# Kernel optimization log

Measured on AMD Instinct MI355X. Metric: run time of the kernel, lower is better.

The kernel has to match this reference:

```python
import jax, jax.numpy as jnp
import numpy as np

E, TOP_K, H, I = 8, 2, 1024, 2048
B, S = 1, 2048


def setup_inputs() -> dict:
    key = jax.random.key(0)
    ks = jax.random.split(key, 5)
    scale_h = 1.0 / np.sqrt(H)
    scale_i = 1.0 / np.sqrt(I)
    return {
        "hidden_states": jax.random.normal(ks[0], (B, S, H), dtype=jnp.float32),
        "gate_w": jax.random.normal(ks[1], (E, H), dtype=jnp.float32) * scale_h,
        "w1": jax.random.normal(ks[2], (E, I, H), dtype=jnp.float32) * scale_h,
        "w3": jax.random.normal(ks[3], (E, I, H), dtype=jnp.float32) * scale_h,
        "w2": jax.random.normal(ks[4], (E, H, I), dtype=jnp.float32) * scale_i,
    }


def _moe(x, gate_w, w1, w3, w2):
    orig_shape = x.shape
    xt = x.reshape(-1, H)                       # [T, H]
    logits = xt @ gate_w.T                      # [T, E] router logits
    probs = jax.nn.softmax(logits, axis=-1)
    topw, topi = jax.lax.top_k(probs, TOP_K)    # [T, K]
    topw = topw / jnp.sum(topw, axis=-1, keepdims=True)  # renormalize=True
    # dense per-token expert weights [T, E]
    ew = jnp.sum(jax.nn.one_hot(topi, E, dtype=xt.dtype) * topw[..., None], axis=1)
    # SwiGLU experts, vectorized over all experts
    g = jnp.einsum('th,eih->tei', xt, w1)       # [T, E, I]
    u = jnp.einsum('th,eih->tei', xt, w3)
    act = jax.nn.silu(g) * u
    ye = jnp.einsum('tei,ehi->teh', act, w2)    # [T, E, H]
    out = jnp.einsum('te,teh->th', ew, ye)      # weighted combine
    return out.reshape(orig_shape)


def reference(hidden_states, gate_w, w1, w3, w2):
    return _moe(hidden_states, gate_w, w1, w3, w2)
```

## Files before the change

kernel.cpp:

```cpp
#include <hip/hip_runtime.h>
#include <hip/hip_bf16.h>
#include <math.h>

#define T_TOK 2048
#define HD 1024
#define ID 2048
#define NE 8
#define LDT 72

typedef __attribute__((ext_vector_type(8))) short s16x8;
typedef __attribute__((ext_vector_type(8))) unsigned short u16x8;
typedef __attribute__((ext_vector_type(4))) float f32x4;
typedef __attribute__((ext_vector_type(4))) unsigned short u16x4;

__device__ __forceinline__ unsigned short f2bf(float f) {
  union { float f; unsigned u; } v; v.f = f;
  unsigned r = v.u + 0x7FFFu + ((v.u >> 16) & 1u);
  return (unsigned short)(r >> 16);
}

__device__ __forceinline__ u16x8 pack8(float4 a, float4 b) {
  u16x8 v;
  v[0] = f2bf(a.x); v[1] = f2bf(a.y); v[2] = f2bf(a.z); v[3] = f2bf(a.w);
  v[4] = f2bf(b.x); v[5] = f2bf(b.y); v[6] = f2bf(b.z); v[7] = f2bf(b.w);
  return v;
}

__device__ __forceinline__ void lgkm_barrier() {
  asm volatile("s_waitcnt lgkmcnt(0)" ::: "memory");
  __builtin_amdgcn_s_barrier();
}

#define GLOAD16(gsrc, ldst) \
  __builtin_amdgcn_global_load_lds((const __attribute__((address_space(1))) void*)(gsrc), \
                                   (__attribute__((address_space(3))) void*)(ldst), 16, 0, 0)

__global__ void router_k(const float* __restrict__ x, const float* __restrict__ gate,
                         int* __restrict__ cnt, int* __restrict__ tok,
                         float* __restrict__ wt, int* __restrict__ inv) {
  int wid = threadIdx.x >> 6, lane = threadIdx.x & 63;
  int t = blockIdx.x * 4 + wid;
  const float* xr = x + (size_t)t * HD;
  float acc[NE];
#pragma unroll
  for (int e = 0; e < NE; e++) acc[e] = 0.f;
  for (int h = lane; h < HD; h += 64) {
    float xv = xr[h];
#pragma unroll
    for (int e = 0; e < NE; e++) acc[e] += xv * gate[e * HD + h];
  }
#pragma unroll
  for (int e = 0; e < NE; e++)
    for (int off = 32; off; off >>= 1) acc[e] += __shfl_xor(acc[e], off);
  int i0 = 0;
#pragma unroll
  for (int e = 1; e < NE; e++) if (acc[e] > acc[i0]) i0 = e;
  int i1 = (i0 == 0) ? 1 : 0;
#pragma unroll
  for (int e = 0; e < NE; e++) if (e != i0 && acc[e] > acc[i1]) i1 = e;
  float w0 = 1.f / (1.f + expf(acc[i1] - acc[i0]));
  float w1 = 1.f - w0;
  if (lane == 0) {
    int p0 = atomicAdd(&cnt[i0], 1);
    tok[i0 * T_TOK + p0] = t; wt[i0 * T_TOK + p0] = w0;
    inv[2 * t] = (i0 << 16) | p0;
    int p1 = atomicAdd(&cnt[i1], 1);
    tok[i1 * T_TOK + p1] = t; wt[i1 * T_TOK + p1] = w1;
    inv[2 * t + 1] = (i1 << 16) | p1;
  }
}

__global__ void prefix_k(const int* __restrict__ cnt, int* __restrict__ offs) {
  if (threadIdx.x == 0) {
    int s = 0;
    for (int e = 0; e < NE; e++) { offs[e] = s; s += cnt[e]; }
  }
}

__global__ void gather_k(const float* __restrict__ x, const int* __restrict__ cnt,
                         const int* __restrict__ offs, const int* __restrict__ tok,
                         unsigned short* __restrict__ Xg) {
  int e = blockIdx.x >> 11, slot = blockIdx.x & 2047;
  if (slot >= cnt[e]) return;
  int t = tok[e * T_TOK + slot];
  int row = offs[e] + slot;
  int c = threadIdx.x * 4;
  float4 f = *(const float4*)(x + (size_t)t * HD + c);
  u16x4 o; o.x = f2bf(f.x); o.y = f2bf(f.y); o.z = f2bf(f.z); o.w = f2bf(f.w);
  *(u16x4*)(Xg + (size_t)row * HD + c) = o;
}

__global__ __launch_bounds__(256, 3) void gemm1_k(
    const unsigned short* __restrict__ Xg, const float* __restrict__ w1,
    const float* __restrict__ w3, const int* __restrict__ cnt,
    const int* __restrict__ offs, const float* __restrict__ wt,
    unsigned short* __restrict__ act) {
  int e = blockIdx.z;
  int count = cnt[e];
  int mt = blockIdx.y;
  if (mt * 128 >= count) return;
  int i0 = blockIdx.x * 64;
  int rbase = offs[e] + mt * 128;
  const float* W1 = w1 + (size_t)e * ID * HD;
  const float* W3 = w3 + (size_t)e * ID * HD;

  __shared__ __align__(16) unsigned short Abuf[2][128 * 64];
  __shared__ __align__(16) unsigned short B1s[64 * LDT];
  __shared__ __align__(16) unsigned short B2s[64 * LDT];

  int tid = threadIdx.x;
  int wid = tid >> 6, lane = tid & 63;
  int wr = wid >> 1, wc = wid & 1;
  int l15 = lane & 15, hi = lane >> 4;
  int br = tid >> 2, bc = (tid & 3) * 16;

  int swz_col = ((lane & 7) ^ (lane >> 3)) * 8;
  const unsigned short* ag[4];
#pragma unroll
  for (int c = 0; c < 4; c++)
    ag[c] = Xg + (size_t)(rbase + c * 32 + wid * 8 + (lane >> 3)) * HD + swz_col;

  const float* s1 = W1 + (size_t)(i0 + br) * HD + bc;
  const float* s2 = W3 + (size_t)(i0 + br) * HD + bc;

  f32x4 accg[4][2], accu[4][2];
#pragma unroll
  for (int m = 0; m < 4; m++)
#pragma unroll
    for (int n = 0; n < 2; n++) {
      accg[m][n] = (f32x4){0.f, 0.f, 0.f, 0.f};
      accu[m][n] = (f32x4){0.f, 0.f, 0.f, 0.f};
    }

#pragma unroll
  for (int c = 0; c < 4; c++) GLOAD16(ag[c], &Abuf[0][c * 2048 + wid * 512]);
  float4 p1[4], p2[4];
#pragma unroll
  for (int j = 0; j < 4; j++) { p1[j] = *(const float4*)(s1 + j * 4); p2[j] = *(const float4*)(s2 + j * 4); }

  for (int t = 0; t < 16; ++t) {
    int cur = t & 1;
    lgkm_barrier();
    *(u16x8*)&B1s[br * LDT + bc]     = pack8(p1[0], p1[1]);
    *(u16x8*)&B1s[br * LDT + bc + 8] = pack8(p1[2], p1[3]);
    *(u16x8*)&B2s[br * LDT + bc]     = pack8(p2[0], p2[1]);
    *(u16x8*)&B2s[br * LDT + bc + 8] = pack8(p2[2], p2[3]);
    lgkm_barrier();
    __builtin_amdgcn_sched_barrier(0);
    if (t < 15) {
      int k0n = (t + 1) * 64;
#pragma unroll
      for (int c = 0; c < 4; c++)
        GLOAD16(ag[c] + k0n, &Abuf[cur ^ 1][c * 2048 + wid * 512]);
#pragma unroll
      for (int j = 0; j < 4; j++) {
        p1[j] = *(const float4*)(s1 + k0n + j * 4);
        p2[j] = *(const float4*)(s2 + k0n + j * 4);
      }
    }
#pragma unroll
    for (int kk = 0; kk < 2; ++kk) {
      s16x8 a[4], b1[2], b2[2];
#pragma unroll
      for (int m = 0; m < 4; m++) {
        int r = wr * 64 + m * 16 + l15;
        a[m] = *(const s16x8*)&Abuf[cur][r * 64 + (((kk * 4 + hi) ^ (r & 7)) * 8)];
      }
#pragma unroll
      for (int n = 0; n < 2; n++) {
        b1[n] = *(const s16x8*)&B1s[(wc * 32 + n * 16 + l15) * LDT + kk * 32 + hi * 8];
        b2[n] = *(const s16x8*)&B2s[(wc * 32 + n * 16 + l15) * LDT + kk * 32 + hi * 8];
      }
#pragma unroll
      for (int m = 0; m < 4; m++)
#pragma unroll
        for (int n = 0; n < 2; n++) {
          accg[m][n] = __builtin_amdgcn_mfma_f32_16x16x32_bf16(a[m], b1[n], accg[m][n], 0, 0, 0);
          accu[m][n] = __builtin_amdgcn_mfma_f32_16x16x32_bf16(a[m], b2[n], accu[m][n], 0, 0, 0);
        }
    }
  }

#pragma unroll
  for (int m = 0; m < 4; m++)
#pragma unroll
    for (int r = 0; r < 4; r++) {
      int rl = mt * 128 + wr * 64 + m * 16 + (lane >> 4) * 4 + r;
      if (rl < count) {
        float w = wt[e * T_TOK + rl];
#pragma unroll
        for (int n = 0; n < 2; n++) {
          float g = accg[m][n][r], u = accu[m][n][r];
          float s = (g / (1.f + expf(-g))) * u * w;
          act[(size_t)(offs[e] + rl) * ID + i0 + wc * 32 + n * 16 + l15] = f2bf(s);
        }
      }
    }
}

__global__ __launch_bounds__(256, 3) void gemm2_k(
    const unsigned short* __restrict__ act, const float* __restrict__ w2,
    const int* __restrict__ cnt, const int* __restrict__ offs,
    float* __restrict__ ye) {
  int e = blockIdx.z;
  int count = cnt[e];
  int mt = blockIdx.y;
  if (mt * 128 >= count) return;
  int h0 = blockIdx.x * 64;
  int rbase = offs[e] + mt * 128;
  const float* W2 = w2 + (size_t)e * HD * ID;

  __shared__ __align__(16) unsigned short Abuf[2][128 * 64];
  __shared__ __align__(16) unsigned short Bs[64 * LDT];

  int tid = threadIdx.x;
  int wid = tid >> 6, lane = tid & 63;
  int wr = wid >> 1, wc = wid & 1;
  int l15 = lane & 15, hi = lane >> 4;
  int br = tid >> 2, bc = (tid & 3) * 16;

  int swz_col = ((lane & 7) ^ (lane >> 3)) * 8;
  const unsigned short* ag[4];
#pragma unroll
  for (int c = 0; c < 4; c++)
    ag[c] = act + (size_t)(rbase + c * 32 + wid * 8 + (lane >> 3)) * ID + swz_col;

  const float* sb = W2 + (size_t)(h0 + br) * ID + bc;

  f32x4 acc[4][2];
#pragma unroll
  for (int m = 0; m < 4; m++)
#pragma unroll
    for (int n = 0; n < 2; n++) acc[m][n] = (f32x4){0.f, 0.f, 0.f, 0.f};

#pragma unroll
  for (int c = 0; c < 4; c++) GLOAD16(ag[c], &Abuf[0][c * 2048 + wid * 512]);
  float4 pb[4];
#pragma unroll
  for (int j = 0; j < 4; j++) pb[j] = *(const float4*)(sb + j * 4);

  for (int t = 0; t < 32; ++t) {
    int cur = t & 1;
    lgkm_barrier();
    *(u16x8*)&Bs[br * LDT + bc]     = pack8(pb[0], pb[1]);
    *(u16x8*)&Bs[br * LDT + bc + 8] = pack8(pb[2], pb[3]);
    lgkm_barrier();
    __builtin_amdgcn_sched_barrier(0);
    if (t < 31) {
      int k0n = (t + 1) * 64;
#pragma unroll
      for (int c = 0; c < 4; c++)
        GLOAD16(ag[c] + k0n, &Abuf[cur ^ 1][c * 2048 + wid * 512]);
#pragma unroll
      for (int j = 0; j < 4; j++) pb[j] = *(const float4*)(sb + k0n + j * 4);
    }
#pragma unroll
    for (int kk = 0; kk < 2; ++kk) {
      s16x8 a[4], b[2];
#pragma unroll
      for (int m = 0; m < 4; m++) {
        int r = wr * 64 + m * 16 + l15;
        a[m] = *(const s16x8*)&Abuf[cur][r * 64 + (((kk * 4 + hi) ^ (r & 7)) * 8)];
      }
#pragma unroll
      for (int n = 0; n < 2; n++)
        b[n] = *(const s16x8*)&Bs[(wc * 32 + n * 16 + l15) * LDT + kk * 32 + hi * 8];
#pragma unroll
      for (int m = 0; m < 4; m++)
#pragma unroll
        for (int n = 0; n < 2; n++)
          acc[m][n] = __builtin_amdgcn_mfma_f32_16x16x32_bf16(a[m], b[n], acc[m][n], 0, 0, 0);
    }
  }

#pragma unroll
  for (int m = 0; m < 4; m++)
#pragma unroll
    for (int r = 0; r < 4; r++) {
      int slot = mt * 128 + wr * 64 + m * 16 + (lane >> 4) * 4 + r;
      if (slot < count) {
#pragma unroll
        for (int n = 0; n < 2; n++)
          ye[(size_t)(offs[e] + slot) * HD + h0 + wc * 32 + n * 16 + l15] = acc[m][n][r];
      }
    }
}

__global__ void combine_k(const float* __restrict__ ye, const int* __restrict__ inv,
                          const int* __restrict__ offs, float* __restrict__ out) {
  int t = blockIdx.x;
  int c = threadIdx.x * 4;
  int v0 = inv[2 * t], v1 = inv[2 * t + 1];
  int r0 = offs[v0 >> 16] + (v0 & 0xFFFF);
  int r1 = offs[v1 >> 16] + (v1 & 0xFFFF);
  float4 a = *(const float4*)(ye + (size_t)r0 * HD + c);
  float4 b = *(const float4*)(ye + (size_t)r1 * HD + c);
  float4 o = {a.x + b.x, a.y + b.y, a.z + b.z, a.w + b.w};
  *(float4*)(out + (size_t)t * HD + c) = o;
}

extern "C" void kernel_launch(void* const* d_in, const int* in_sizes, int n_in,
                              void* d_out, int out_size, void* d_ws, size_t ws_size,
                              hipStream_t stream) {
  const float* x    = (const float*)d_in[0];
  const float* gate = (const float*)d_in[1];
  const float* w1   = (const float*)d_in[2];
  const float* w3   = (const float*)d_in[3];
  const float* w2   = (const float*)d_in[4];
  float* out = (float*)d_out;

  char* ws = (char*)d_ws;
  int* cnt  = (int*)(ws + 0);
  int* offs = (int*)(ws + 256);
  int* tok  = (int*)(ws + 512);
  float* wt = (float*)(ws + 66048);
  int* inv  = (int*)(ws + 131584);
  unsigned short* Xg  = (unsigned short*)(ws + 148480);
  unsigned short* act = (unsigned short*)(ws + 8799232);
  float* ye = (float*)(ws + 26100736);

  hipMemsetAsync(cnt, 0, 256, stream);

  router_k<<<T_TOK / 4, 256, 0, stream>>>(x, gate, cnt, tok, wt, inv);
  prefix_k<<<1, 64, 0, stream>>>(cnt, offs);
  gather_k<<<NE * T_TOK, 256, 0, stream>>>(x, cnt, offs, tok, Xg);
  gemm1_k<<<dim3(ID / 64, 16, NE), 256, 0, stream>>>(Xg, w1, w3, cnt, offs, wt, act);
  gemm2_k<<<dim3(HD / 64, 16, NE), 256, 0, stream>>>(act, w2, cnt, offs, ye);
  combine_k<<<T_TOK, 256, 0, stream>>>(ye, inv, offs, out);
}
```

Before: 371.1 us.

## Stream fp32 expert weights into LDS asynchronously and enlarge M tiles

Both expert GEMMs now move fp32 weight tiles straight into shared memory with asynchronous global-to-LDS loads, using an XOR swizzle, and convert them to bf16 when the fragments are read. Previously the weights went through registers and were packed to bf16 before an LDS store. Blocks grow to 512 threads covering 256 token rows with a K step of 32, and the grid is flattened with experts interleaved in the block index. Each weight tile is therefore re-read fewer times and the register round trip leaves the inner loop. In exchange each wave converts fp32 to bf16 redundantly, barriers become more frequent, and the grid assumes at most 1024 tokens per expert.

```diff
diff --git a/kernel.cpp b/kernel.cpp
--- a/kernel.cpp
+++ b/kernel.cpp
@@ -6,7 +6,6 @@
 #define HD 1024
 #define ID 2048
 #define NE 8
-#define LDT 72
 
 typedef __attribute__((ext_vector_type(8))) short s16x8;
 typedef __attribute__((ext_vector_type(8))) unsigned short u16x8;
@@ -19,21 +18,22 @@
   return (unsigned short)(r >> 16);
 }
 
-__device__ __forceinline__ u16x8 pack8(float4 a, float4 b) {
-  u16x8 v;
-  v[0] = f2bf(a.x); v[1] = f2bf(a.y); v[2] = f2bf(a.z); v[3] = f2bf(a.w);
-  v[4] = f2bf(b.x); v[5] = f2bf(b.y); v[6] = f2bf(b.z); v[7] = f2bf(b.w);
-  return v;
-}
-
-__device__ __forceinline__ void lgkm_barrier() {
-  asm volatile("s_waitcnt lgkmcnt(0)" ::: "memory");
-  __builtin_amdgcn_s_barrier();
+__device__ __forceinline__ s16x8 cvt8(float4 a, float4 b) {
+  union { s16x8 v; __hip_bfloat16 h[8]; } u;
+  u.h[0] = __float2bfloat16(a.x); u.h[1] = __float2bfloat16(a.y);
+  u.h[2] = __float2bfloat16(a.z); u.h[3] = __float2bfloat16(a.w);
+  u.h[4] = __float2bfloat16(b.x); u.h[5] = __float2bfloat16(b.y);
+  u.h[6] = __float2bfloat16(b.z); u.h[7] = __float2bfloat16(b.w);
+  return u.v;
 }
 
 #define GLOAD16(gsrc, ldst) \
   __builtin_amdgcn_global_load_lds((const __attribute__((address_space(1))) void*)(gsrc), \
                                    (__attribute__((address_space(3))) void*)(ldst), 16, 0, 0)
+
+#define WAIT_BARRIER() do { \
+  asm volatile("s_waitcnt vmcnt(0) lgkmcnt(0)" ::: "memory"); \
+  __builtin_amdgcn_s_barrier(); } while (0)
 
 __global__ void router_k(const float* __restrict__ x, const float* __restrict__ gate,
                          int* __restrict__ cnt, int* __restrict__ tok,
@@ -90,38 +90,40 @@
   *(u16x4*)(Xg + (size_t)row * HD + c) = o;
 }
 
-__global__ __launch_bounds__(256, 3) void gemm1_k(
+__global__ __launch_bounds__(512, 4) void gemm1_k(
     const unsigned short* __restrict__ Xg, const float* __restrict__ w1,
     const float* __restrict__ w3, const int* __restrict__ cnt,
     const int* __restrict__ offs, const float* __restrict__ wt,
     unsigned short* __restrict__ act) {
-  int e = blockIdx.z;
+  int bid = blockIdx.x;
+  int e = bid & 7;
+  int r2 = bid >> 3;
+  int nt = r2 & 31, mt = r2 >> 5;
   int count = cnt[e];
-  int mt = blockIdx.y;
-  if (mt * 128 >= count) return;
-  int i0 = blockIdx.x * 64;
-  int rbase = offs[e] + mt * 128;
+  if (mt * 256 >= count) return;
+  int i0 = nt * 64;
+  int rbase = offs[e] + mt * 256;
   const float* W1 = w1 + (size_t)e * ID * HD;
   const float* W3 = w3 + (size_t)e * ID * HD;
 
-  __shared__ __align__(16) unsigned short Abuf[2][128 * 64];
-  __shared__ __align__(16) unsigned short B1s[64 * LDT];
-  __shared__ __align__(16) unsigned short B2s[64 * LDT];
+  __shared__ __align__(16) unsigned short Ab[2][256 * 32];
+  __shared__ __align__(16) float B1b[2][64 * 32];
+  __shared__ __align__(16) float B2b[2][64 * 32];
 
   int tid = threadIdx.x;
   int wid = tid >> 6, lane = tid & 63;
   int wr = wid >> 1, wc = wid & 1;
   int l15 = lane & 15, hi = lane >> 4;
-  int br = tid >> 2, bc = (tid & 3) * 16;
-
-  int swz_col = ((lane & 7) ^ (lane >> 3)) * 8;
-  const unsigned short* ag[4];
-#pragma unroll
-  for (int c = 0; c < 4; c++)
-    ag[c] = Xg + (size_t)(rbase + c * 32 + wid * 8 + (lane >> 3)) * HD + swz_col;
-
-  const float* s1 = W1 + (size_t)(i0 + br) * HD + bc;
-  const float* s2 = W3 + (size_t)(i0 + br) * HD + bc;
+
+  const unsigned short* aS[2];
+#pragma unroll
+  for (int c = 0; c < 2; c++)
+    aS[c] = Xg + (size_t)(rbase + c * 128 + wid * 16 + (lane >> 2)) * HD
+               + (((lane & 3) ^ ((lane >> 2) & 3)) * 8);
+  const float* b1S = W1 + (size_t)(i0 + wid * 8 + (lane >> 3)) * HD
+                        + (((lane & 7) ^ ((lane >> 3) & 7)) * 4);
+  const float* b2S = W3 + (size_t)(i0 + wid * 8 + (lane >> 3)) * HD
+                        + (((lane & 7) ^ ((lane >> 3) & 7)) * 4);
 
   f32x4 accg[4][2], accu[4][2];
 #pragma unroll
@@ -132,100 +134,92 @@
       accu[m][n] = (f32x4){0.f, 0.f, 0.f, 0.f};
     }
 
-#pragma unroll
-  for (int c = 0; c < 4; c++) GLOAD16(ag[c], &Abuf[0][c * 2048 + wid * 512]);
-  float4 p1[4], p2[4];
-#pragma unroll
-  for (int j = 0; j < 4; j++) { p1[j] = *(const float4*)(s1 + j * 4); p2[j] = *(const float4*)(s2 + j * 4); }
-
-  for (int t = 0; t < 16; ++t) {
+  int aswz = (hi ^ (l15 & 3)) * 8;
+  int bg0 = ((hi * 2) ^ (l15 & 7)) * 4;
+  int bg1 = ((hi * 2 + 1) ^ (l15 & 7)) * 4;
+
+#define G1_STAGE(buf, k0) do { \
+    GLOAD16(aS[0] + (k0), &Ab[buf][wid * 512]); \
+    GLOAD16(aS[1] + (k0), &Ab[buf][4096 + wid * 512]); \
+    GLOAD16(b1S + (k0), &B1b[buf][wid * 256]); \
+    GLOAD16(b2S + (k0), &B2b[buf][wid * 256]); } while (0)
+
+  G1_STAGE(0, 0);
+  WAIT_BARRIER();
+
+  for (int t = 0; t < 32; ++t) {
     int cur = t & 1;
-    lgkm_barrier();
-    *(u16x8*)&B1s[br * LDT + bc]     = pack8(p1[0], p1[1]);
-    *(u16x8*)&B1s[br * LDT + bc + 8] = pack8(p1[2], p1[3]);
-    *(u16x8*)&B2s[br * LDT + bc]     = pack8(p2[0], p2[1]);
-    *(u16x8*)&B2s[br * LDT + bc + 8] = pack8(p2[2], p2[3]);
-    lgkm_barrier();
-    __builtin_amdgcn_sched_barrier(0);
-    if (t < 15) {
-      int k0n = (t + 1) * 64;
-#pragma unroll
-      for (int c = 0; c < 4; c++)
-        GLOAD16(ag[c] + k0n, &Abuf[cur ^ 1][c * 2048 + wid * 512]);
-#pragma unroll
-      for (int j = 0; j < 4; j++) {
-        p1[j] = *(const float4*)(s1 + k0n + j * 4);
-        p2[j] = *(const float4*)(s2 + k0n + j * 4);
+    if (t < 31) G1_STAGE(cur ^ 1, (t + 1) * 32);
+    s16x8 a[4];
+#pragma unroll
+    for (int m = 0; m < 4; m++)
+      a[m] = *(const s16x8*)&Ab[cur][(wr * 64 + m * 16 + l15) * 32 + aswz];
+#pragma unroll
+    for (int n = 0; n < 2; n++) {
+      int rB = (wc * 32 + n * 16 + l15) * 32;
+      float4 q0 = *(const float4*)&B1b[cur][rB + bg0];
+      float4 q1 = *(const float4*)&B1b[cur][rB + bg1];
+      s16x8 b1 = cvt8(q0, q1);
+      float4 q2 = *(const float4*)&B2b[cur][rB + bg0];
+      float4 q3 = *(const float4*)&B2b[cur][rB + bg1];
+      s16x8 b2 = cvt8(q2, q3);
+#pragma unroll
+      for (int m = 0; m < 4; m++) {
+        accg[m][n] = __builtin_amdgcn_mfma_f32_16x16x32_bf16(a[m], b1, accg[m][n], 0, 0, 0);
+        accu[m][n] = __builtin_amdgcn_mfma_f32_16x16x32_bf16(a[m], b2, accu[m][n], 0, 0, 0);
       }
     }
-#pragma unroll
-    for (int kk = 0; kk < 2; ++kk) {
-      s16x8 a[4], b1[2], b2[2];
-#pragma unroll
-      for (int m = 0; m < 4; m++) {
-        int r = wr * 64 + m * 16 + l15;
-        a[m] = *(const s16x8*)&Abuf[cur][r * 64 + (((kk * 4 + hi) ^ (r & 7)) * 8)];
-      }
-#pragma unroll
-      for (int n = 0; n < 2; n++) {
-        b1[n] = *(const s16x8*)&B1s[(wc * 32 + n * 16 + l15) * LDT + kk * 32 + hi * 8];
-        b2[n] = *(const s16x8*)&B2s[(wc * 32 + n * 16 + l15) * LDT + kk * 32 + hi * 8];
-      }
-#pragma unroll
-      for (int m = 0; m < 4; m++)
-#pragma unroll
-        for (int n = 0; n < 2; n++) {
-          accg[m][n] = __builtin_amdgcn_mfma_f32_16x16x32_bf16(a[m], b1[n], accg[m][n], 0, 0, 0);
-          accu[m][n] = __builtin_amdgcn_mfma_f32_16x16x32_bf16(a[m], b2[n], accu[m][n], 0, 0, 0);
-        }
-    }
+    WAIT_BARRIER();
   }
 
 #pragma unroll
   for (int m = 0; m < 4; m++)
 #pragma unroll
     for (int r = 0; r < 4; r++) {
-      int rl = mt * 128 + wr * 64 + m * 16 + (lane >> 4) * 4 + r;
+      int rl = mt * 256 + wr * 64 + m * 16 + hi * 4 + r;
       if (rl < count) {
         float w = wt[e * T_TOK + rl];
 #pragma unroll
         for (int n = 0; n < 2; n++) {
           float g = accg[m][n][r], u = accu[m][n][r];
           float s = (g / (1.f + expf(-g))) * u * w;
-          act[(size_t)(offs[e] + rl) * ID + i0 + wc * 32 + n * 16 + l15] = f2bf(s);
+          act[(size_t)(offs[e] + rl) * ID + i0 + wc * 32 + n * 16 + l15] =
+              (unsigned short)__bfloat16_as_ushort(__float2bfloat16(s));
         }
       }
     }
-}
-
-__global__ __launch_bounds__(256, 3) void gemm2_k(
+#undef G1_STAGE
+}
+
+__global__ __launch_bounds__(512, 4) void gemm2_k(
     const unsigned short* __restrict__ act, const float* __restrict__ w2,
     const int* __restrict__ cnt, const int* __restrict__ offs,
     float* __restrict__ ye) {
-  int e = blockIdx.z;
+  int bid = blockIdx.x;
+  int e = bid & 7;
+  int r2 = bid >> 3;
+  int nt = r2 & 15, mt = r2 >> 4;
   int count = cnt[e];
-  int mt = blockIdx.y;
-  if (mt * 128 >= count) return;
-  int h0 = blockIdx.x * 64;
-  int rbase = offs[e] + mt * 128;
+  if (mt * 256 >= count) return;
+  int h0 = nt * 64;
+  int rbase = offs[e] + mt * 256;
   const float* W2 = w2 + (size_t)e * HD * ID;
 
-  __shared__ __align__(16) unsigned short Abuf[2][128 * 64];
-  __shared__ __align__(16) unsigned short Bs[64 * LDT];
+  __shared__ __align__(16) unsigned short Ab[2][256 * 32];
+  __shared__ __align__(16) float Bb[2][64 * 32];
 
   int tid = threadIdx.x;
   int wid = tid >> 6, lane = tid & 63;
   int wr = wid >> 1, wc = wid & 1;
   int l15 = lane & 15, hi = lane >> 4;
-  int br = tid >> 2, bc = (tid & 3) * 16;
-
-  int swz_col = ((lane & 7) ^ (lane >> 3)) * 8;
-  const unsigned short* ag[4];
-#pragma unroll
-  for (int c = 0; c < 4; c++)
-    ag[c] = act + (size_t)(rbase + c * 32 + wid * 8 + (lane >> 3)) * ID + swz_col;
-
-  const float* sb = W2 + (size_t)(h0 + br) * ID + bc;
+
+  const unsigned short* aS[2];
+#pragma unroll
+  for (int c = 0; c < 2; c++)
+    aS[c] = act + (size_t)(rbase + c * 128 + wid * 16 + (lane >> 2)) * ID
+                + (((lane & 3) ^ ((lane >> 2) & 3)) * 8);
+  const float* bS = W2 + (size_t)(h0 + wid * 8 + (lane >> 3)) * ID
+                       + (((lane & 7) ^ ((lane >> 3) & 7)) * 4);
 
   f32x4 acc[4][2];
 #pragma unroll
@@ -233,57 +227,50 @@
 #pragma unroll
     for (int n = 0; n < 2; n++) acc[m][n] = (f32x4){0.f, 0.f, 0.f, 0.f};
 
-#pragma unroll
-  for (int c = 0; c < 4; c++) GLOAD16(ag[c], &Abuf[0][c * 2048 + wid * 512]);
-  float4 pb[4];
-#pragma unroll
-  for (int j = 0; j < 4; j++) pb[j] = *(const float4*)(sb + j * 4);
-
-  for (int t = 0; t < 32; ++t) {
+  int aswz = (hi ^ (l15 & 3)) * 8;
+  int bg0 = ((hi * 2) ^ (l15 & 7)) * 4;
+  int bg1 = ((hi * 2 + 1) ^ (l15 & 7)) * 4;
+
+#define G2_STAGE(buf, k0) do { \
+    GLOAD16(aS[0] + (k0), &Ab[buf][wid * 512]); \
+    GLOAD16(aS[1] + (k0), &Ab[buf][4096 + wid * 512]); \
+    GLOAD16(bS + (k0), &Bb[buf][wid * 256]); } while (0)
+
+  G2_STAGE(0, 0);
+  WAIT_BARRIER();
+
+  for (int t = 0; t < 64; ++t) {
     int cur = t & 1;
-    lgkm_barrier();
-    *(u16x8*)&Bs[br * LDT + bc]     = pack8(pb[0], pb[1]);
-    *(u16x8*)&Bs[br * LDT + bc + 8] = pack8(pb[2], pb[3]);
-    lgkm_barrier();
-    __builtin_amdgcn_sched_barrier(0);
-    if (t < 31) {
-      int k0n = (t + 1) * 64;
-#pragma unroll
-      for (int c = 0; c < 4; c++)
-        GLOAD16(ag[c] + k0n, &Abuf[cur ^ 1][c * 2048 + wid * 512]);
-#pragma unroll
-      for (int j = 0; j < 4; j++) pb[j] = *(const float4*)(sb + k0n + j * 4);
-    }
-#pragma unroll
-    for (int kk = 0; kk < 2; ++kk) {
-      s16x8 a[4], b[2];
-#pragma unroll
-      for (int m = 0; m < 4; m++) {
-        int r = wr * 64 + m * 16 + l15;
-        a[m] = *(const s16x8*)&Abuf[cur][r * 64 + (((kk * 4 + hi) ^ (r & 7)) * 8)];
-      }
-#pragma unroll
-      for (int n = 0; n < 2; n++)
-        b[n] = *(const s16x8*)&Bs[(wc * 32 + n * 16 + l15) * LDT + kk * 32 + hi * 8];
+    if (t < 63) G2_STAGE(cur ^ 1, (t + 1) * 32);
+    s16x8 a[4];
+#pragma unroll
+    for (int m = 0; m < 4; m++)
+      a[m] = *(const s16x8*)&Ab[cur][(wr * 64 + m * 16 + l15) * 32 + aswz];
+#pragma unroll
+    for (int n = 0; n < 2; n++) {
+      int rB = (wc * 32 + n * 16 + l15) * 32;
+      float4 q0 = *(const float4*)&Bb[cur][rB + bg0];
+      float4 q1 = *(const float4*)&Bb[cur][rB + bg1];
+      s16x8 b = cvt8(q0, q1);
 #pragma unroll
       for (int m = 0; m < 4; m++)
-#pragma unroll
-        for (int n = 0; n < 2; n++)
-          acc[m][n] = __builtin_amdgcn_mfma_f32_16x16x32_bf16(a[m], b[n], acc[m][n], 0, 0, 0);
-    }
+        acc[m][n] = __builtin_amdgcn_mfma_f32_16x16x32_bf16(a[m], b, acc[m][n], 0, 0, 0);
+    }
+    WAIT_BARRIER();
   }
 
 #pragma unroll
   for (int m = 0; m < 4; m++)
 #pragma unroll
     for (int r = 0; r < 4; r++) {
-      int slot = mt * 128 + wr * 64 + m * 16 + (lane >> 4) * 4 + r;
+      int slot = mt * 256 + wr * 64 + m * 16 + hi * 4 + r;
       if (slot < count) {
 #pragma unroll
         for (int n = 0; n < 2; n++)
           ye[(size_t)(offs[e] + slot) * HD + h0 + wc * 32 + n * 16 + l15] = acc[m][n][r];
       }
     }
+#undef G2_STAGE
 }
 
 __global__ void combine_k(const float* __restrict__ ye, const int* __restrict__ inv,
@@ -316,15 +303,15 @@
   float* wt = (float*)(ws + 66048);
   int* inv  = (int*)(ws + 131584);
   unsigned short* Xg  = (unsigned short*)(ws + 148480);
-  unsigned short* act = (unsigned short*)(ws + 8799232);
-  float* ye = (float*)(ws + 26100736);
+  unsigned short* act = (unsigned short*)(ws + 10634240);
+  float* ye = (float*)(ws + 31605760);
 
   hipMemsetAsync(cnt, 0, 256, stream);
 
   router_k<<<T_TOK / 4, 256, 0, stream>>>(x, gate, cnt, tok, wt, inv);
   prefix_k<<<1, 64, 0, stream>>>(cnt, offs);
   gather_k<<<NE * T_TOK, 256, 0, stream>>>(x, cnt, offs, tok, Xg);
-  gemm1_k<<<dim3(ID / 64, 16, NE), 256, 0, stream>>>(Xg, w1, w3, cnt, offs, wt, act);
-  gemm2_k<<<dim3(HD / 64, 16, NE), 256, 0, stream>>>(act, w2, cnt, offs, ye);
+  gemm1_k<<<NE * 32 * 4, 512, 0, stream>>>(Xg, w1, w3, cnt, offs, wt, act);
+  gemm2_k<<<NE * 16 * 4, 512, 0, stream>>>(act, w2, cnt, offs, ye);
   combine_k<<<T_TOK, 256, 0, stream>>>(ye, inv, offs, out);
 }
```

Measured after the change: 405.4 us. 9.3% more time.

## Restructure grouped GEMMs with register-staged K=32 pipeline and split-K for down projection

Applied to the files above, without the earlier changes.

Both expert GEMMs drop the async global-to-LDS loads and instead stage operands through registers. They use K-steps of 32, a triple-buffered B tile and a double-buffered A tile, with one barrier per step instead of two. Blocks now come from a flattened 1-D grid with experts interleaved in the low bits, which spreads the expert loads across the device. The down-projection GEMM is split along K into two halves written to separate buffers, and the combine kernel sums the four partial rows. This adds a second ye buffer and more combine traffic, and the narrower K step doubles the barrier count per unit of work.

```diff
diff --git a/kernel.cpp b/kernel.cpp
--- a/kernel.cpp
+++ b/kernel.cpp
@@ -6,7 +6,7 @@
 #define HD 1024
 #define ID 2048
 #define NE 8
-#define LDT 72
+#define LDA 36
 
 typedef __attribute__((ext_vector_type(8))) short s16x8;
 typedef __attribute__((ext_vector_type(8))) unsigned short u16x8;
@@ -26,14 +26,10 @@
   return v;
 }
 
-__device__ __forceinline__ void lgkm_barrier() {
-  asm volatile("s_waitcnt lgkmcnt(0)" ::: "memory");
-  __builtin_amdgcn_s_barrier();
-}
-
-#define GLOAD16(gsrc, ldst) \
-  __builtin_amdgcn_global_load_lds((const __attribute__((address_space(1))) void*)(gsrc), \
-                                   (__attribute__((address_space(3))) void*)(ldst), 16, 0, 0)
+#define PHASE_BARRIER() do { \
+  asm volatile("s_waitcnt lgkmcnt(0)" ::: "memory"); \
+  __builtin_amdgcn_s_barrier(); \
+  __builtin_amdgcn_sched_barrier(0); } while (0)
 
 __global__ void router_k(const float* __restrict__ x, const float* __restrict__ gate,
                          int* __restrict__ cnt, int* __restrict__ tok,
@@ -95,33 +91,39 @@
     const float* __restrict__ w3, const int* __restrict__ cnt,
     const int* __restrict__ offs, const float* __restrict__ wt,
     unsigned short* __restrict__ act) {
-  int e = blockIdx.z;
+  int bid = blockIdx.x;
+  int e = bid & 7;
+  int r2 = bid >> 3;
+  int nt = r2 & 31, mt = r2 >> 5;
   int count = cnt[e];
-  int mt = blockIdx.y;
   if (mt * 128 >= count) return;
-  int i0 = blockIdx.x * 64;
+  int i0 = nt * 64;
   int rbase = offs[e] + mt * 128;
   const float* W1 = w1 + (size_t)e * ID * HD;
   const float* W3 = w3 + (size_t)e * ID * HD;
 
-  __shared__ __align__(16) unsigned short Abuf[2][128 * 64];
-  __shared__ __align__(16) unsigned short B1s[64 * LDT];
-  __shared__ __align__(16) unsigned short B2s[64 * LDT];
+  __shared__ __align__(16) unsigned short Ab[2][128 * LDA];
+  __shared__ __align__(16) unsigned short B1b[3][64 * LDA];
+  __shared__ __align__(16) unsigned short B2b[3][64 * LDA];
 
   int tid = threadIdx.x;
   int wid = tid >> 6, lane = tid & 63;
   int wr = wid >> 1, wc = wid & 1;
   int l15 = lane & 15, hi = lane >> 4;
-  int br = tid >> 2, bc = (tid & 3) * 16;
-
-  int swz_col = ((lane & 7) ^ (lane >> 3)) * 8;
-  const unsigned short* ag[4];
-#pragma unroll
-  for (int c = 0; c < 4; c++)
-    ag[c] = Xg + (size_t)(rbase + c * 32 + wid * 8 + (lane >> 3)) * HD + swz_col;
-
-  const float* s1 = W1 + (size_t)(i0 + br) * HD + bc;
-  const float* s2 = W3 + (size_t)(i0 + br) * HD + bc;
+
+  int rowA = tid >> 1, colA = (tid & 1) * 16;
+  const unsigned short* aSrc = Xg + (size_t)(rbase + rowA) * HD + colA;
+  int aDst = rowA * LDA + colA;
+  int rowB = tid >> 2, colB = (tid & 3) * 8;
+  const float* s1 = W1 + (size_t)(i0 + rowB) * HD + colB;
+  const float* s2 = W3 + (size_t)(i0 + rowB) * HD + colB;
+  int bDst = rowB * LDA + colB;
+
+  int aOff[4], bOff[2];
+#pragma unroll
+  for (int m = 0; m < 4; m++) aOff[m] = (wr * 64 + m * 16 + l15) * LDA + hi * 8;
+#pragma unroll
+  for (int n = 0; n < 2; n++) bOff[n] = (wc * 32 + n * 16 + l15) * LDA + hi * 8;
 
   f32x4 accg[4][2], accu[4][2];
 #pragma unroll
@@ -132,60 +134,86 @@
       accu[m][n] = (f32x4){0.f, 0.f, 0.f, 0.f};
     }
 
-#pragma unroll
-  for (int c = 0; c < 4; c++) GLOAD16(ag[c], &Abuf[0][c * 2048 + wid * 512]);
-  float4 p1[4], p2[4];
-#pragma unroll
-  for (int j = 0; j < 4; j++) { p1[j] = *(const float4*)(s1 + j * 4); p2[j] = *(const float4*)(s2 + j * 4); }
-
-  for (int t = 0; t < 16; ++t) {
-    int cur = t & 1;
-    lgkm_barrier();
-    *(u16x8*)&B1s[br * LDT + bc]     = pack8(p1[0], p1[1]);
-    *(u16x8*)&B1s[br * LDT + bc + 8] = pack8(p1[2], p1[3]);
-    *(u16x8*)&B2s[br * LDT + bc]     = pack8(p2[0], p2[1]);
-    *(u16x8*)&B2s[br * LDT + bc + 8] = pack8(p2[2], p2[3]);
-    lgkm_barrier();
-    __builtin_amdgcn_sched_barrier(0);
-    if (t < 15) {
-      int k0n = (t + 1) * 64;
-#pragma unroll
-      for (int c = 0; c < 4; c++)
-        GLOAD16(ag[c] + k0n, &Abuf[cur ^ 1][c * 2048 + wid * 512]);
-#pragma unroll
-      for (int j = 0; j < 4; j++) {
-        p1[j] = *(const float4*)(s1 + k0n + j * 4);
-        p2[j] = *(const float4*)(s2 + k0n + j * 4);
-      }
-    }
-#pragma unroll
-    for (int kk = 0; kk < 2; ++kk) {
-      s16x8 a[4], b1[2], b2[2];
-#pragma unroll
-      for (int m = 0; m < 4; m++) {
-        int r = wr * 64 + m * 16 + l15;
-        a[m] = *(const s16x8*)&Abuf[cur][r * 64 + (((kk * 4 + hi) ^ (r & 7)) * 8)];
-      }
-#pragma unroll
-      for (int n = 0; n < 2; n++) {
-        b1[n] = *(const s16x8*)&B1s[(wc * 32 + n * 16 + l15) * LDT + kk * 32 + hi * 8];
-        b2[n] = *(const s16x8*)&B2s[(wc * 32 + n * 16 + l15) * LDT + kk * 32 + hi * 8];
-      }
-#pragma unroll
-      for (int m = 0; m < 4; m++)
-#pragma unroll
-        for (int n = 0; n < 2; n++) {
-          accg[m][n] = __builtin_amdgcn_mfma_f32_16x16x32_bf16(a[m], b1[n], accg[m][n], 0, 0, 0);
-          accu[m][n] = __builtin_amdgcn_mfma_f32_16x16x32_bf16(a[m], b2[n], accu[m][n], 0, 0, 0);
-        }
-    }
-  }
+  u16x8 tA0 = *(const u16x8*)aSrc, tA1 = *(const u16x8*)(aSrc + 8);
+  float4 q10 = *(const float4*)s1, q11 = *(const float4*)(s1 + 4);
+  float4 q20 = *(const float4*)s2, q21 = *(const float4*)(s2 + 4);
+  *(u16x8*)&Ab[0][aDst] = tA0; *(u16x8*)&Ab[0][aDst + 8] = tA1;
+  *(u16x8*)&B1b[0][bDst] = pack8(q10, q11);
+  *(u16x8*)&B2b[0][bDst] = pack8(q20, q21);
+  u16x8 ar1a = *(const u16x8*)(aSrc + 32), ar1b = *(const u16x8*)(aSrc + 40);
+  float4 b1x0 = *(const float4*)(s1 + 32), b1y0 = *(const float4*)(s1 + 36);
+  float4 b2x0 = *(const float4*)(s2 + 32), b2y0 = *(const float4*)(s2 + 36);
+  float4 b1x1 = *(const float4*)(s1 + 64), b1y1 = *(const float4*)(s1 + 68);
+  float4 b2x1 = *(const float4*)(s2 + 64), b2y1 = *(const float4*)(s2 + 68);
+  u16x8 ar0a, ar0b;
+  PHASE_BARRIER();
+
+#define G1_COMPUTE(AB, BB) do { \
+    s16x8 a_[4], f1_[2], f2_[2]; \
+    _Pragma("unroll") \
+    for (int m = 0; m < 4; m++) a_[m] = *(const s16x8*)&Ab[AB][aOff[m]]; \
+    _Pragma("unroll") \
+    for (int n = 0; n < 2; n++) { \
+      f1_[n] = *(const s16x8*)&B1b[BB][bOff[n]]; \
+      f2_[n] = *(const s16x8*)&B2b[BB][bOff[n]]; \
+    } \
+    _Pragma("unroll") \
+    for (int m = 0; m < 4; m++) \
+      _Pragma("unroll") \
+      for (int n = 0; n < 2; n++) { \
+        accg[m][n] = __builtin_amdgcn_mfma_f32_16x16x32_bf16(a_[m], f1_[n], accg[m][n], 0, 0, 0); \
+        accu[m][n] = __builtin_amdgcn_mfma_f32_16x16x32_bf16(a_[m], f2_[n], accu[m][n], 0, 0, 0); \
+      } \
+  } while (0)
+
+  int cur = 0;
+  for (int tt = 0; tt < 32; tt += 2) {
+    {
+      int t = tt;
+      int wb = cur + 1; if (wb == 3) wb = 0;
+      *(u16x8*)&Ab[1][aDst] = ar1a; *(u16x8*)&Ab[1][aDst + 8] = ar1b;
+      *(u16x8*)&B1b[wb][bDst] = pack8(b1x0, b1y0);
+      *(u16x8*)&B2b[wb][bDst] = pack8(b2x0, b2y0);
+      if (t + 2 < 32) {
+        ar0a = *(const u16x8*)(aSrc + (t + 2) * 32);
+        ar0b = *(const u16x8*)(aSrc + (t + 2) * 32 + 8);
+      }
+      if (t + 3 < 32) {
+        b1x0 = *(const float4*)(s1 + (t + 3) * 32); b1y0 = *(const float4*)(s1 + (t + 3) * 32 + 4);
+        b2x0 = *(const float4*)(s2 + (t + 3) * 32); b2y0 = *(const float4*)(s2 + (t + 3) * 32 + 4);
+      }
+      G1_COMPUTE(0, cur);
+      PHASE_BARRIER();
+      cur = wb;
+    }
+    {
+      int t = tt + 1;
+      int wb = cur + 1; if (wb == 3) wb = 0;
+      if (t + 1 < 32) {
+        *(u16x8*)&Ab[0][aDst] = ar0a; *(u16x8*)&Ab[0][aDst + 8] = ar0b;
+        *(u16x8*)&B1b[wb][bDst] = pack8(b1x1, b1y1);
+        *(u16x8*)&B2b[wb][bDst] = pack8(b2x1, b2y1);
+      }
+      if (t + 2 < 32) {
+        ar1a = *(const u16x8*)(aSrc + (t + 2) * 32);
+        ar1b = *(const u16x8*)(aSrc + (t + 2) * 32 + 8);
+      }
+      if (t + 3 < 32) {
+        b1x1 = *(const float4*)(s1 + (t + 3) * 32); b1y1 = *(const float4*)(s1 + (t + 3) * 32 + 4);
+        b2x1 = *(const float4*)(s2 + (t + 3) * 32); b2y1 = *(const float4*)(s2 + (t + 3) * 32 + 4);
+      }
+      G1_COMPUTE(1, cur);
+      PHASE_BARRIER();
+      cur = wb;
+    }
+  }
+#undef G1_COMPUTE
 
 #pragma unroll
   for (int m = 0; m < 4; m++)
 #pragma unroll
     for (int r = 0; r < 4; r++) {
-      int rl = mt * 128 + wr * 64 + m * 16 + (lane >> 4) * 4 + r;
+      int rl = mt * 128 + wr * 64 + m * 16 + hi * 4 + r;
       if (rl < count) {
         float w = wt[e * T_TOK + rl];
 #pragma unroll
@@ -198,34 +226,44 @@
     }
 }
 
-__global__ __launch_bounds__(256, 3) void gemm2_k(
+__global__ __launch_bounds__(256, 4) void gemm2_k(
     const unsigned short* __restrict__ act, const float* __restrict__ w2,
     const int* __restrict__ cnt, const int* __restrict__ offs,
-    float* __restrict__ ye) {
-  int e = blockIdx.z;
+    float* __restrict__ ye0, float* __restrict__ ye1) {
+  int bid = blockIdx.x;
+  int e = bid & 7;
+  int r2 = bid >> 3;
+  int nt = r2 & 15;
+  int mt = (r2 >> 4) & 15;
+  int split = r2 >> 8;
   int count = cnt[e];
-  int mt = blockIdx.y;
   if (mt * 128 >= count) return;
-  int h0 = blockIdx.x * 64;
+  int h0 = nt * 64;
+  int kbase = split * 1024;
   int rbase = offs[e] + mt * 128;
   const float* W2 = w2 + (size_t)e * HD * ID;
-
-  __shared__ __align__(16) unsigned short Abuf[2][128 * 64];
-  __shared__ __align__(16) unsigned short Bs[64 * LDT];
+  float* ye = split ? ye1 : ye0;
+
+  __shared__ __align__(16) unsigned short Ab[2][128 * LDA];
+  __shared__ __align__(16) unsigned short Bb[3][64 * LDA];
 
   int tid = threadIdx.x;
   int wid = tid >> 6, lane = tid & 63;
   int wr = wid >> 1, wc = wid & 1;
   int l15 = lane & 15, hi = lane >> 4;
-  int br = tid >> 2, bc = (tid & 3) * 16;
-
-  int swz_col = ((lane & 7) ^ (lane >> 3)) * 8;
-  const unsigned short* ag[4];
-#pragma unroll
-  for (int c = 0; c < 4; c++)
-    ag[c] = act + (size_t)(rbase + c * 32 + wid * 8 + (lane >> 3)) * ID + swz_col;
-
-  const float* sb = W2 + (size_t)(h0 + br) * ID + bc;
+
+  int rowA = tid >> 1, colA = (tid & 1) * 16;
+  const unsigned short* aSrc = act + (size_t)(rbase + rowA) * ID + kbase + colA;
+  int aDst = rowA * LDA + colA;
+  int rowB = tid >> 2, colB = (tid & 3) * 8;
+  const float* sB = W2 + (size_t)(h0 + rowB) * ID + kbase + colB;
+  int bDst = rowB * LDA + colB;
+
+  int aOff[4], bOff[2];
+#pragma unroll
+  for (int m = 0; m < 4; m++) aOff[m] = (wr * 64 + m * 16 + l15) * LDA + hi * 8;
+#pragma unroll
+  for (int n = 0; n < 2; n++) bOff[n] = (wc * 32 + n * 16 + l15) * LDA + hi * 8;
 
   f32x4 acc[4][2];
 #pragma unroll
@@ -233,51 +271,73 @@
 #pragma unroll
     for (int n = 0; n < 2; n++) acc[m][n] = (f32x4){0.f, 0.f, 0.f, 0.f};
 
-#pragma unroll
-  for (int c = 0; c < 4; c++) GLOAD16(ag[c], &Abuf[0][c * 2048 + wid * 512]);
-  float4 pb[4];
-#pragma unroll
-  for (int j = 0; j < 4; j++) pb[j] = *(const float4*)(sb + j * 4);
-
-  for (int t = 0; t < 32; ++t) {
-    int cur = t & 1;
-    lgkm_barrier();
-    *(u16x8*)&Bs[br * LDT + bc]     = pack8(pb[0], pb[1]);
-    *(u16x8*)&Bs[br * LDT + bc + 8] = pack8(pb[2], pb[3]);
-    lgkm_barrier();
-    __builtin_amdgcn_sched_barrier(0);
-    if (t < 31) {
-      int k0n = (t + 1) * 64;
-#pragma unroll
-      for (int c = 0; c < 4; c++)
-        GLOAD16(ag[c] + k0n, &Abuf[cur ^ 1][c * 2048 + wid * 512]);
-#pragma unroll
-      for (int j = 0; j < 4; j++) pb[j] = *(const float4*)(sb + k0n + j * 4);
-    }
-#pragma unroll
-    for (int kk = 0; kk < 2; ++kk) {
-      s16x8 a[4], b[2];
-#pragma unroll
-      for (int m = 0; m < 4; m++) {
-        int r = wr * 64 + m * 16 + l15;
-        a[m] = *(const s16x8*)&Abuf[cur][r * 64 + (((kk * 4 + hi) ^ (r & 7)) * 8)];
-      }
-#pragma unroll
-      for (int n = 0; n < 2; n++)
-        b[n] = *(const s16x8*)&Bs[(wc * 32 + n * 16 + l15) * LDT + kk * 32 + hi * 8];
-#pragma unroll
-      for (int m = 0; m < 4; m++)
-#pragma unroll
-        for (int n = 0; n < 2; n++)
-          acc[m][n] = __builtin_amdgcn_mfma_f32_16x16x32_bf16(a[m], b[n], acc[m][n], 0, 0, 0);
-    }
-  }
+  u16x8 tA0 = *(const u16x8*)aSrc, tA1 = *(const u16x8*)(aSrc + 8);
+  float4 q0 = *(const float4*)sB, q1 = *(const float4*)(sB + 4);
+  *(u16x8*)&Ab[0][aDst] = tA0; *(u16x8*)&Ab[0][aDst + 8] = tA1;
+  *(u16x8*)&Bb[0][bDst] = pack8(q0, q1);
+  u16x8 ar1a = *(const u16x8*)(aSrc + 32), ar1b = *(const u16x8*)(aSrc + 40);
+  float4 bx0 = *(const float4*)(sB + 32), by0 = *(const float4*)(sB + 36);
+  float4 bx1 = *(const float4*)(sB + 64), by1 = *(const float4*)(sB + 68);
+  u16x8 ar0a, ar0b;
+  PHASE_BARRIER();
+
+#define G2_COMPUTE(AB, BB) do { \
+    s16x8 a_[4], f_[2]; \
+    _Pragma("unroll") \
+    for (int m = 0; m < 4; m++) a_[m] = *(const s16x8*)&Ab[AB][aOff[m]]; \
+    _Pragma("unroll") \
+    for (int n = 0; n < 2; n++) f_[n] = *(const s16x8*)&Bb[BB][bOff[n]]; \
+    _Pragma("unroll") \
+    for (int m = 0; m < 4; m++) \
+      _Pragma("unroll") \
+      for (int n = 0; n < 2; n++) \
+        acc[m][n] = __builtin_amdgcn_mfma_f32_16x16x32_bf16(a_[m], f_[n], acc[m][n], 0, 0, 0); \
+  } while (0)
+
+  int cur = 0;
+  for (int tt = 0; tt < 32; tt += 2) {
+    {
+      int t = tt;
+      int wb = cur + 1; if (wb == 3) wb = 0;
+      *(u16x8*)&Ab[1][aDst] = ar1a; *(u16x8*)&Ab[1][aDst + 8] = ar1b;
+      *(u16x8*)&Bb[wb][bDst] = pack8(bx0, by0);
+      if (t + 2 < 32) {
+        ar0a = *(const u16x8*)(aSrc + (t + 2) * 32);
+        ar0b = *(const u16x8*)(aSrc + (t + 2) * 32 + 8);
+      }
+      if (t + 3 < 32) {
+        bx0 = *(const float4*)(sB + (t + 3) * 32); by0 = *(const float4*)(sB + (t + 3) * 32 + 4);
+      }
+      G2_COMPUTE(0, cur);
+      PHASE_BARRIER();
+      cur = wb;
+    }
+    {
+      int t = tt + 1;
+      int wb = cur + 1; if (wb == 3) wb = 0;
+      if (t + 1 < 32) {
+        *(u16x8*)&Ab[0][aDst] = ar0a; *(u16x8*)&Ab[0][aDst + 8] = ar0b;
+        *(u16x8*)&Bb[wb][bDst] = pack8(bx1, by1);
+      }
+      if (t + 2 < 32) {
+        ar1a = *(const u16x8*)(aSrc + (t + 2) * 32);
+        ar1b = *(const u16x8*)(aSrc + (t + 2) * 32 + 8);
+      }
+      if (t + 3 < 32) {
+        bx1 = *(const float4*)(sB + (t + 3) * 32); by1 = *(const float4*)(sB + (t + 3) * 32 + 4);
+      }
+      G2_COMPUTE(1, cur);
+      PHASE_BARRIER();
+      cur = wb;
+    }
+  }
+#undef G2_COMPUTE
 
 #pragma unroll
   for (int m = 0; m < 4; m++)
 #pragma unroll
     for (int r = 0; r < 4; r++) {
-      int slot = mt * 128 + wr * 64 + m * 16 + (lane >> 4) * 4 + r;
+      int slot = mt * 128 + wr * 64 + m * 16 + hi * 4 + r;
       if (slot < count) {
 #pragma unroll
         for (int n = 0; n < 2; n++)
@@ -286,16 +346,20 @@
     }
 }
 
-__global__ void combine_k(const float* __restrict__ ye, const int* __restrict__ inv,
-                          const int* __restrict__ offs, float* __restrict__ out) {
+__global__ void combine_k(const float* __restrict__ ye0, const float* __restrict__ ye1,
+                          const int* __restrict__ inv, const int* __restrict__ offs,
+                          float* __restrict__ out) {
   int t = blockIdx.x;
   int c = threadIdx.x * 4;
   int v0 = inv[2 * t], v1 = inv[2 * t + 1];
-  int r0 = offs[v0 >> 16] + (v0 & 0xFFFF);
-  int r1 = offs[v1 >> 16] + (v1 & 0xFFFF);
-  float4 a = *(const float4*)(ye + (size_t)r0 * HD + c);
-  float4 b = *(const float4*)(ye + (size_t)r1 * HD + c);
-  float4 o = {a.x + b.x, a.y + b.y, a.z + b.z, a.w + b.w};
+  size_t r0 = (size_t)(offs[v0 >> 16] + (v0 & 0xFFFF)) * HD + c;
+  size_t r1 = (size_t)(offs[v1 >> 16] + (v1 & 0xFFFF)) * HD + c;
+  float4 a0 = *(const float4*)(ye0 + r0);
+  float4 a1 = *(const float4*)(ye1 + r0);
+  float4 b0 = *(const float4*)(ye0 + r1);
+  float4 b1 = *(const float4*)(ye1 + r1);
+  float4 o = {a0.x + a1.x + b0.x + b1.x, a0.y + a1.y + b0.y + b1.y,
+              a0.z + a1.z + b0.z + b1.z, a0.w + a1.w + b0.w + b1.w};
   *(float4*)(out + (size_t)t * HD + c) = o;
 }
 
@@ -316,15 +380,16 @@
   float* wt = (float*)(ws + 66048);
   int* inv  = (int*)(ws + 131584);
   unsigned short* Xg  = (unsigned short*)(ws + 148480);
-  unsigned short* act = (unsigned short*)(ws + 8799232);
-  float* ye = (float*)(ws + 26100736);
+  unsigned short* act = (unsigned short*)(ws + 10634240);
+  float* ye0 = (float*)(ws + 31605760);
+  float* ye1 = (float*)(ws + 48907264);
 
   hipMemsetAsync(cnt, 0, 256, stream);
 
   router_k<<<T_TOK / 4, 256, 0, stream>>>(x, gate, cnt, tok, wt, inv);
   prefix_k<<<1, 64, 0, stream>>>(cnt, offs);
   gather_k<<<NE * T_TOK, 256, 0, stream>>>(x, cnt, offs, tok, Xg);
-  gemm1_k<<<dim3(ID / 64, 16, NE), 256, 0, stream>>>(Xg, w1, w3, cnt, offs, wt, act);
-  gemm2_k<<<dim3(HD / 64, 16, NE), 256, 0, stream>>>(act, w2, cnt, offs, ye);
-  combine_k<<<T_TOK, 256, 0, stream>>>(ye, inv, offs, out);
-}
+  gemm1_k<<<NE * 32 * 16, 256, 0, stream>>>(Xg, w1, w3, cnt, offs, wt, act);
+  gemm2_k<<<NE * 16 * 16 * 2, 256, 0, stream>>>(act, w2, cnt, offs, ye0, ye1);
+  combine_k<<<T_TOK, 256, 0, stream>>>(ye0, ye1, inv, offs, out);
+}
```

Result: slower. 390.9 us (+5.3%).
